# Optimization experiments

Measured on AMD Instinct MI355X. Metric: run time of the kernel, lower is better.

Reference implementation:

```python
import jax, jax.numpy as jnp
import numpy as np

N_NODES = 50000
N_EDGES = 800000
D = 128          # embed_dim
H = 8            # heads
C = D // H       # per-head channels
F = 512          # ff_hidden_dim
LN_EPS = 1e-5
NEG_SLOPE = 0.2  # PyG GATConv default negative_slope


def _layernorm(x, g, b):
    mu = jnp.mean(x, axis=-1, keepdims=True)
    var = jnp.mean(jnp.square(x - mu), axis=-1, keepdims=True)
    return (x - mu) * jax.lax.rsqrt(var + LN_EPS) * g + b


def _gat_conv(x, edge_index, W, att_src, att_dst, bias):
    # PyG GATConv (concat=True, add_self_loops=True, shared lin for src/dst)
    N = x.shape[0]
    xl = (x @ W.T).reshape(N, H, C)                 # [N,H,C]
    a_s = jnp.sum(xl * att_src, axis=-1)            # [N,H]
    a_d = jnp.sum(xl * att_dst, axis=-1)            # [N,H]
    loops = jnp.arange(N)
    src = jnp.concatenate([edge_index[0], loops])   # [E+N]
    dst = jnp.concatenate([edge_index[1], loops])
    e = jax.nn.leaky_relu(a_s[src] + a_d[dst], NEG_SLOPE)  # [E+N,H]
    # segment softmax over incoming edges per destination node
    m = jax.ops.segment_max(e, dst, num_segments=N)
    m = jnp.where(jnp.isfinite(m), m, jnp.zeros_like(m))
    ex = jnp.exp(e - m[dst])
    s = jax.ops.segment_sum(ex, dst, num_segments=N)
    alpha = ex / (s[dst] + 1e-16)                   # [E+N,H]
    msg = xl[src] * alpha[:, :, None]               # [E+N,H,C]
    out = jax.ops.segment_sum(msg, dst, num_segments=N)  # [N,H,C]
    return out.reshape(N, H * C) + bias


def setup_inputs() -> dict:
    key = jax.random.key(0)
    ks = jax.random.split(key, 12)
    sc_d = 1.0 / np.sqrt(D)
    sc_f = 1.0 / np.sqrt(F)
    return {
        "x": jax.random.normal(ks[0], (N_NODES, D), dtype=jnp.float32),
        "virtual_edge_index": jax.random.randint(ks[1], (2, N_EDGES), 0, N_NODES, dtype=jnp.int64),
        "W_gat": jax.random.normal(ks[2], (H * C, D), dtype=jnp.float32) * sc_d,
        "att_src": jax.random.normal(ks[3], (H, C), dtype=jnp.float32) * sc_d,
        "att_dst": jax.random.normal(ks[4], (H, C), dtype=jnp.float32) * sc_d,
        "bias_gat": jnp.zeros((H * C,), dtype=jnp.float32),
        "W1": jax.random.normal(ks[5], (F, D), dtype=jnp.float32) * sc_d,
        "b1": jnp.zeros((F,), dtype=jnp.float32),
        "W2": jax.random.normal(ks[6], (D, F), dtype=jnp.float32) * sc_f,
        "b2": jnp.zeros((D,), dtype=jnp.float32),
        "g1": jnp.ones((D,), dtype=jnp.float32),
        "beta1": jnp.zeros((D,), dtype=jnp.float32),
        "g2": jnp.ones((D,), dtype=jnp.float32),
        "beta2": jnp.zeros((D,), dtype=jnp.float32),
    }


def reference(x, virtual_edge_index, W_gat, att_src, att_dst, bias_gat,
              W1, b1, W2, b2, g1, beta1, g2, beta2):
    h_gat = _gat_conv(x, virtual_edge_index, W_gat, att_src, att_dst, bias_gat)
    h = _layernorm(x + h_gat, g1, beta1)
    h_ff = jax.nn.relu(h @ W1.T + b1) @ W2.T + b2
    return _layernorm(h + h_ff, g2, beta2)
```

## Files before the change

kernel.cpp:

```cpp
#include <hip/hip_runtime.h>
#include <hip/hip_bf16.h>

#define N_NODES 50000
#define N_EDGES 800000
#define N_TOT   850000
#define DIM 128
#define HEADS 8
#define CH 16
#define FF 512
#define LN_EPS 1e-5f
#define NEG_SLOPE 0.2f

typedef __bf16 bf16x8 __attribute__((ext_vector_type(8)));
typedef float f32x4 __attribute__((ext_vector_type(4)));

__device__ __forceinline__ float bfr2f(unsigned short u) {
  return __uint_as_float(((unsigned)u) << 16);
}
__device__ __forceinline__ unsigned short f2bfr(float f) {
  __hip_bfloat16 h = __float2bfloat16(f);
  return *(unsigned short*)&h;
}
__device__ __forceinline__ float bf2f(__hip_bfloat16 h) { return __bfloat162float(h); }
__device__ __forceinline__ __hip_bfloat16 f2bf(float f) { return __float2bfloat16(f); }

__device__ __forceinline__ bf16x8 ldcvt8(const float* __restrict__ p) {
  const float4 a = ((const float4*)p)[0];
  const float4 b = ((const float4*)p)[1];
  bf16x8 r;
  r[0] = (__bf16)a.x; r[1] = (__bf16)a.y; r[2] = (__bf16)a.z; r[3] = (__bf16)a.w;
  r[4] = (__bf16)b.x; r[5] = (__bf16)b.y; r[6] = (__bf16)b.z; r[7] = (__bf16)b.w;
  return r;
}
__device__ __forceinline__ void load8f(const float* __restrict__ p, float* v) {
  const float4 a = ((const float4*)p)[0];
  const float4 b = ((const float4*)p)[1];
  v[0]=a.x; v[1]=a.y; v[2]=a.z; v[3]=a.w; v[4]=b.x; v[5]=b.y; v[6]=b.z; v[7]=b.w;
}

__device__ __forceinline__ int ld_src(const int* ei, int mode, int e) {
  int v = mode ? ei[2 * e] : ei[e];
  return min(max(v, 0), N_NODES - 1);
}
__device__ __forceinline__ int ld_dst(const int* ei, int mode, int e) {
  int v = mode ? ei[2 * (N_EDGES + e)] : ei[N_EDGES + e];
  return min(max(v, 0), N_NODES - 1);
}

__global__ __launch_bounds__(256) void k_setup(const float* __restrict__ Wg,
                                               const float* __restrict__ W1,
                                               const float* __restrict__ W2,
                                               __hip_bfloat16* __restrict__ wb,
                                               const int* __restrict__ ei,
                                               int* __restrict__ flag,
                                               int* __restrict__ dz) {
  int i = blockIdx.x * 256 + threadIdx.x;
  if (i < 16384)       wb[i] = f2bf(Wg[i]);
  else if (i < 81920)  wb[i] = f2bf(W1[i - 16384]);
  else if (i < 147456) wb[i] = f2bf(W2[i - 81920]);
  if (i < 100096) dz[i] = 0;
  if (i == 0) {
    int any = 0;
    for (int k = 1; k < 64; k += 2) any |= ei[k];
    *flag = (any == 0) ? 1 : 0;
  }
}

__global__ __launch_bounds__(256) void k_xl(const float* __restrict__ x,
                                            const __hip_bfloat16* __restrict__ Wgb,
                                            __hip_bfloat16* __restrict__ xl) {
  int w = (blockIdx.x * blockDim.x + threadIdx.x) >> 6;
  if (w >= 3125 * 2) return;
  int l = threadIdx.x & 63, quad = l >> 4, r = l & 15;
  int strip = w >> 1, cc = w & 1;
  const __bf16* wb = (const __bf16*)Wgb;
  f32x4 acc[4];
#pragma unroll
  for (int t = 0; t < 4; ++t) acc[t] = (f32x4){0.f, 0.f, 0.f, 0.f};
  int arow = strip * 16 + r;
  bf16x8 af[4];
#pragma unroll
  for (int kk = 0; kk < 4; ++kk) af[kk] = ldcvt8(x + arow * DIM + kk * 32 + quad * 8);
#pragma unroll
  for (int kk = 0; kk < 4; ++kk) {
    bf16x8 bfr[4];
#pragma unroll
    for (int t = 0; t < 4; ++t)
      bfr[t] = *(const bf16x8*)(wb + (cc * 64 + t * 16 + r) * DIM + kk * 32 + quad * 8);
#pragma unroll
    for (int t = 0; t < 4; ++t)
      acc[t] = __builtin_amdgcn_mfma_f32_16x16x32_bf16(af[kk], bfr[t], acc[t], 0, 0, 0);
  }
#pragma unroll
  for (int t = 0; t < 4; ++t)
#pragma unroll
    for (int j = 0; j < 4; ++j) {
      int row = strip * 16 + quad * 4 + j;
      int col = cc * 64 + t * 16 + r;
      xl[row * DIM + col] = f2bf(acc[t][j]);
    }
}

__global__ __launch_bounds__(256) void k_score(const __hip_bfloat16* __restrict__ xl,
                                               const float* __restrict__ att_s,
                                               const float* __restrict__ att_d,
                                               float* __restrict__ a_s, float* __restrict__ a_d) {
  int t = blockIdx.x * 256 + threadIdx.x;
  if (t >= N_NODES * HEADS) return;
  int n = t >> 3, h = t & 7;
  const __hip_bfloat16* p = xl + n * DIM + h * CH;
  float s = 0.f, d = 0.f;
#pragma unroll
  for (int c = 0; c < CH; ++c) {
    float v = bf2f(p[c]);
    s += v * att_s[h * CH + c];
    d += v * att_d[h * CH + c];
  }
  a_s[t] = s; a_d[t] = d;
}

__global__ __launch_bounds__(256) void k_hist(const int* __restrict__ ei, const int* __restrict__ flag,
                                              int* __restrict__ deg) {
  int e = blockIdx.x * 256 + threadIdx.x;
  if (e < N_EDGES) atomicAdd(&deg[ld_dst(ei, *flag, e)], 1);
}

__global__ __launch_bounds__(1024) void k_scan(const int* __restrict__ deg, int* __restrict__ offs) {
  __shared__ int wtot[16];
  __shared__ int wbase[16];
  __shared__ int running_s;
  int tid = threadIdx.x, wv = tid >> 6, ln = tid & 63;
  if (tid == 0) running_s = 0;
  __syncthreads();
  for (int base = 0; base < N_NODES; base += 4096) {
    int i0 = base + tid * 4;
    int v0 = 0, v1 = 0, v2 = 0, v3 = 0;
    if (i0 + 3 < N_NODES) {
      int4 dv = *(const int4*)(deg + i0);
      v0 = dv.x + 1; v1 = dv.y + 1; v2 = dv.z + 1; v3 = dv.w + 1;
    } else {
      if (i0 + 0 < N_NODES) v0 = deg[i0 + 0] + 1;
      if (i0 + 1 < N_NODES) v1 = deg[i0 + 1] + 1;
      if (i0 + 2 < N_NODES) v2 = deg[i0 + 2] + 1;
      if (i0 + 3 < N_NODES) v3 = deg[i0 + 3] + 1;
    }
    int tt = v0 + v1 + v2 + v3;
    int xsc = tt;
#pragma unroll
    for (int off = 1; off < 64; off <<= 1) {
      int t = __shfl_up(xsc, off);
      if (ln >= off) xsc += t;
    }
    if (ln == 63) wtot[wv] = xsc;
    __syncthreads();
    if (wv == 0) {
      int t = (ln < 16) ? wtot[ln] : 0;
#pragma unroll
      for (int off = 1; off < 16; off <<= 1) {
        int u = __shfl_up(t, off);
        if (ln >= off) t += u;
      }
      if (ln < 16) wbase[ln] = t;
    }
    __syncthreads();
    int run0 = running_s;
    int excl = run0 + ((wv == 0) ? 0 : wbase[wv - 1]) + xsc - tt;
    if (i0 + 0 < N_NODES) offs[i0 + 0] = excl;
    excl += v0;
    if (i0 + 1 < N_NODES) offs[i0 + 1] = excl;
    excl += v1;
    if (i0 + 2 < N_NODES) offs[i0 + 2] = excl;
    excl += v2;
    if (i0 + 3 < N_NODES) offs[i0 + 3] = excl;
    __syncthreads();
    if (tid == 1023) running_s = run0 + wbase[15];
  }
  __syncthreads();
  if (tid == 0) offs[N_NODES] = running_s;
}

__global__ __launch_bounds__(256) void k_scatter(const int* __restrict__ ei, const int* __restrict__ flag,
                                                 const int* __restrict__ offs,
                                                 int* __restrict__ fill, int* __restrict__ eid,
                                                 int* __restrict__ did) {
  int e = blockIdx.x * 256 + threadIdx.x;
  if (e < N_NODES) { int p = offs[e]; eid[p] = e; did[p] = e; }
  if (e < N_EDGES) {
    int m = *flag;
    int d = ld_dst(ei, m, e);
    int p = offs[d] + 1 + atomicAdd(&fill[d], 1);
    eid[p] = ld_src(ei, m, e);
    did[p] = d;
  }
}

__global__ __launch_bounds__(256) void k_escore(const int* __restrict__ eid, const int* __restrict__ did,
                                                const float* __restrict__ a_s, const float* __restrict__ a_d,
                                                unsigned short* __restrict__ ex) {
  int p = blockIdx.x * 256 + threadIdx.x;
  if (p >= N_TOT) return;
  int s = eid[p], d = did[p];
  float as8[8], ad8[8];
  load8f(a_s + s * 8, as8);
  load8f(a_d + d * 8, ad8);
  unsigned int o[4];
#pragma unroll
  for (int k = 0; k < 4; ++k) {
    float v0 = as8[2 * k] + ad8[2 * k];
    v0 = v0 > 0.f ? v0 : NEG_SLOPE * v0;
    float v1 = as8[2 * k + 1] + ad8[2 * k + 1];
    v1 = v1 > 0.f ? v1 : NEG_SLOPE * v1;
    unsigned short e0 = f2bfr(__expf(v0));
    unsigned short e1 = f2bfr(__expf(v1));
    o[k] = (unsigned)e0 | ((unsigned)e1 << 16);
  }
  *(uint4*)(ex + p * 8) = make_uint4(o[0], o[1], o[2], o[3]);
}

__global__ __launch_bounds__(256) void k_attn(const int* __restrict__ eid, const int* __restrict__ offs,
                                              const unsigned short* __restrict__ ex,
                                              const __hip_bfloat16* __restrict__ xl,
                                              const float* __restrict__ x,
                                              const float* __restrict__ bias,
                                              const float* __restrict__ g1,
                                              const float* __restrict__ be1,
                                              __hip_bfloat16* __restrict__ h1out) {
  int wv = threadIdx.x >> 6, l = threadIdx.x & 63;
  int n = blockIdx.x * 4 + wv;
  int start = offs[n], end = offs[n + 1];

  float sme = 0.f;
  int flat1 = end * 8;
  for (int q = start * 8 + l; q < flat1; q += 64) sme += bfr2f(ex[q]);
  sme += __shfl_xor(sme, 8);
  sme += __shfl_xor(sme, 16);
  sme += __shfl_xor(sme, 32);
  float smh = __shfl(sme, l >> 3);
  float inv = 1.f / (smh + 1e-16f);

  int h = l >> 3;
  const unsigned short* xlu = (const unsigned short*)xl;
  float A0 = 0.f, A1 = 0.f, B0 = 0.f, B1 = 0.f, C0 = 0.f, C1 = 0.f, D0 = 0.f, D1 = 0.f;
  int p = start;
  for (; p + 4 <= end; p += 4) {
    int s0 = eid[p], s1 = eid[p + 1], s2 = eid[p + 2], s3 = eid[p + 3];
    float w0 = bfr2f(ex[(p)     * 8 + h]);
    float w1 = bfr2f(ex[(p + 1) * 8 + h]);
    float w2 = bfr2f(ex[(p + 2) * 8 + h]);
    float w3 = bfr2f(ex[(p + 3) * 8 + h]);
    ushort2 u0 = *(const ushort2*)(xlu + s0 * DIM + 2 * l);
    ushort2 u1 = *(const ushort2*)(xlu + s1 * DIM + 2 * l);
    ushort2 u2 = *(const ushort2*)(xlu + s2 * DIM + 2 * l);
    ushort2 u3 = *(const ushort2*)(xlu + s3 * DIM + 2 * l);
    A0 += w0 * bfr2f(u0.x); A1 += w0 * bfr2f(u0.y);
    B0 += w1 * bfr2f(u1.x); B1 += w1 * bfr2f(u1.y);
    C0 += w2 * bfr2f(u2.x); C1 += w2 * bfr2f(u2.y);
    D0 += w3 * bfr2f(u3.x); D1 += w3 * bfr2f(u3.y);
  }
  for (; p < end; ++p) {
    int s = eid[p];
    float wq = bfr2f(ex[p * 8 + h]);
    ushort2 u = *(const ushort2*)(xlu + s * DIM + 2 * l);
    A0 += wq * bfr2f(u.x); A1 += wq * bfr2f(u.y);
  }
  float acc0 = ((A0 + B0) + (C0 + D0)) * inv;
  float acc1 = ((A1 + B1) + (C1 + D1)) * inv;

  float2 xv = *(const float2*)(x + n * DIM + 2 * l);
  float2 bv = *(const float2*)(bias + 2 * l);
  float v0 = acc0 + bv.x + xv.x;
  float v1 = acc1 + bv.y + xv.y;
  float s2 = v0 + v1;
  for (int off = 32; off >= 1; off >>= 1) s2 += __shfl_xor(s2, off);
  float mu = s2 * (1.f / 128.f);
  float d0 = v0 - mu, d1 = v1 - mu;
  float q = d0 * d0 + d1 * d1;
  for (int off = 32; off >= 1; off >>= 1) q += __shfl_xor(q, off);
  float rs = rsqrtf(q * (1.f / 128.f) + LN_EPS);
  float2 gv = *(const float2*)(g1 + 2 * l);
  float2 bev = *(const float2*)(be1 + 2 * l);
  ushort2 o;
  o.x = f2bfr(d0 * rs * gv.x + bev.x);
  o.y = f2bfr(d1 * rs * gv.y + bev.y);
  *(ushort2*)((unsigned short*)h1out + n * DIM + 2 * l) = o;
}

#define LDSP 520
__global__ __launch_bounds__(256) void k_ffn(const __hip_bfloat16* __restrict__ h1,
                                             const __hip_bfloat16* __restrict__ W1b,
                                             const float* __restrict__ b1,
                                             const __hip_bfloat16* __restrict__ W2b,
                                             const float* __restrict__ b2,
                                             const float* __restrict__ g2,
                                             const float* __restrict__ be2,
                                             float* __restrict__ out) {
  __shared__ __bf16 hid[32 * LDSP];
  __shared__ float ps[4][2][16], pq[4][2][16];
  int wv = threadIdx.x >> 6, l = threadIdx.x & 63, quad = l >> 4, r = l & 15;
  int base = blockIdx.x * 32;
  const __bf16* h1b = (const __bf16*)h1;
  const __bf16* w1 = (const __bf16*)W1b;
  const __bf16* w2 = (const __bf16*)W2b;

  bf16x8 bn[2][4];
#pragma unroll
  for (int kk = 0; kk < 4; ++kk) {
    bn[0][kk] = *(const bf16x8*)(h1b + (base + r) * DIM + kk * 32 + quad * 8);
    bn[1][kk] = *(const bf16x8*)(h1b + (base + 16 + r) * DIM + kk * 32 + quad * 8);
  }
  f32x4 acc1[8][2];
#pragma unroll
  for (int tm = 0; tm < 8; ++tm)
#pragma unroll
    for (int tn = 0; tn < 2; ++tn) acc1[tm][tn] = (f32x4){0.f, 0.f, 0.f, 0.f};
#pragma unroll
  for (int kk = 0; kk < 4; ++kk) {
    bf16x8 wf[8];
#pragma unroll
    for (int tm = 0; tm < 8; ++tm)
      wf[tm] = *(const bf16x8*)(w1 + (wv * 128 + tm * 16 + r) * DIM + kk * 32 + quad * 8);
#pragma unroll
    for (int tm = 0; tm < 8; ++tm) {
      acc1[tm][0] = __builtin_amdgcn_mfma_f32_16x16x32_bf16(wf[tm], bn[0][kk], acc1[tm][0], 0, 0, 0);
      acc1[tm][1] = __builtin_amdgcn_mfma_f32_16x16x32_bf16(wf[tm], bn[1][kk], acc1[tm][1], 0, 0, 0);
    }
  }
#pragma unroll
  for (int tm = 0; tm < 8; ++tm) {
    int f0 = wv * 128 + tm * 16 + quad * 4;
    float4 bb = *(const float4*)(b1 + f0);
#pragma unroll
    for (int tn = 0; tn < 2; ++tn) {
      int node = tn * 16 + r;
      ushort4 o;
      o.x = f2bfr(fmaxf(acc1[tm][tn][0] + bb.x, 0.f));
      o.y = f2bfr(fmaxf(acc1[tm][tn][1] + bb.y, 0.f));
      o.z = f2bfr(fmaxf(acc1[tm][tn][2] + bb.z, 0.f));
      o.w = f2bfr(fmaxf(acc1[tm][tn][3] + bb.w, 0.f));
      *(ushort4*)&hid[node * LDSP + f0] = o;
    }
  }
  __syncthreads();

  f32x4 acc2[2][2];
#pragma unroll
  for (int s = 0; s < 2; ++s)
#pragma unroll
    for (int tn = 0; tn < 2; ++tn) acc2[s][tn] = (f32x4){0.f, 0.f, 0.f, 0.f};
#pragma unroll
  for (int k2 = 0; k2 < 8; ++k2) {
    int ka = 2 * k2, kb = 2 * k2 + 1;
    bf16x8 a0 = *(const bf16x8*)&hid[(r) * LDSP + ka * 32 + quad * 8];
    bf16x8 a1 = *(const bf16x8*)&hid[(16 + r) * LDSP + ka * 32 + quad * 8];
    bf16x8 a0b = *(const bf16x8*)&hid[(r) * LDSP + kb * 32 + quad * 8];
    bf16x8 a1b = *(const bf16x8*)&hid[(16 + r) * LDSP + kb * 32 + quad * 8];
    bf16x8 wa[2], wbq[2];
#pragma unroll
    for (int tn = 0; tn < 2; ++tn) {
      wa[tn]  = *(const bf16x8*)(w2 + (wv * 32 + tn * 16 + r) * FF + ka * 32 + quad * 8);
      wbq[tn] = *(const bf16x8*)(w2 + (wv * 32 + tn * 16 + r) * FF + kb * 32 + quad * 8);
    }
#pragma unroll
    for (int tn = 0; tn < 2; ++tn) {
      acc2[0][tn] = __builtin_amdgcn_mfma_f32_16x16x32_bf16(a0, wa[tn], acc2[0][tn], 0, 0, 0);
      acc2[1][tn] = __builtin_amdgcn_mfma_f32_16x16x32_bf16(a1, wa[tn], acc2[1][tn], 0, 0, 0);
    }
#pragma unroll
    for (int tn = 0; tn < 2; ++tn) {
      acc2[0][tn] = __builtin_amdgcn_mfma_f32_16x16x32_bf16(a0b, wbq[tn], acc2[0][tn], 0, 0, 0);
      acc2[1][tn] = __builtin_amdgcn_mfma_f32_16x16x32_bf16(a1b, wbq[tn], acc2[1][tn], 0, 0, 0);
    }
  }
#pragma unroll
  for (int s = 0; s < 2; ++s)
#pragma unroll
    for (int tn = 0; tn < 2; ++tn) {
      int col = wv * 32 + tn * 16 + r;
      float b2c = b2[col];
#pragma unroll
      for (int j = 0; j < 4; ++j)
        acc2[s][tn][j] += b2c + bf2f(h1[(base + s * 16 + quad * 4 + j) * DIM + col]);
    }
#pragma unroll
  for (int s = 0; s < 2; ++s)
#pragma unroll
    for (int j = 0; j < 4; ++j) {
      float sm = acc2[s][0][j] + acc2[s][1][j];
      float qm = acc2[s][0][j] * acc2[s][0][j] + acc2[s][1][j] * acc2[s][1][j];
      sm += __shfl_xor(sm, 1); sm += __shfl_xor(sm, 2); sm += __shfl_xor(sm, 4); sm += __shfl_xor(sm, 8);
      qm += __shfl_xor(qm, 1); qm += __shfl_xor(qm, 2); qm += __shfl_xor(qm, 4); qm += __shfl_xor(qm, 8);
      if (r == j) { ps[wv][s][quad * 4 + j] = sm; pq[wv][s][quad * 4 + j] = qm; }
    }
  __syncthreads();
#pragma unroll
  for (int s = 0; s < 2; ++s)
#pragma unroll
    for (int j = 0; j < 4; ++j) {
      int row16 = quad * 4 + j;
      float st = (ps[0][s][row16] + ps[1][s][row16]) + (ps[2][s][row16] + ps[3][s][row16]);
      float qt = (pq[0][s][row16] + pq[1][s][row16]) + (pq[2][s][row16] + pq[3][s][row16]);
      float mu = st * (1.f / 128.f);
      float var = qt * (1.f / 128.f) - mu * mu;
      float rs = rsqrtf(var + LN_EPS);
      int grow = base + s * 16 + row16;
      if (grow < N_NODES) {
#pragma unroll
        for (int tn = 0; tn < 2; ++tn) {
          int col = wv * 32 + tn * 16 + r;
          out[grow * DIM + col] = (acc2[s][tn][j] - mu) * rs * g2[col] + be2[col];
        }
      }
    }
}

#define OFF_XL     0u
#define SZ_XL      (N_NODES * DIM * 2u)
#define OFF_AS     (OFF_XL + SZ_XL)
#define SZ_AS      (N_NODES * HEADS * 4u)
#define OFF_AD     (OFF_AS + SZ_AS)
#define OFF_DEG    (OFF_AD + SZ_AS)
#define SZ_DEG     200192u
#define OFF_FILL   (OFF_DEG + SZ_DEG)
#define OFF_OFFS   (OFF_FILL + SZ_DEG)
#define SZ_OFFS    200448u
#define OFF_FLAG   (OFF_OFFS + SZ_OFFS)
#define OFF_EID    (OFF_FLAG + 256u)
#define SZ_EID     3400192u
#define OFF_DID    (OFF_EID + SZ_EID)
#define OFF_EX     (OFF_DID + SZ_EID)
#define SZ_EX      13600768u
#define OFF_H1     (OFF_EX + SZ_EX)
#define SZ_H1      (50016u * DIM * 2u)
#define OFF_WB     (OFF_H1 + SZ_H1)

extern "C" void kernel_launch(void* const* d_in, const int* in_sizes, int n_in,
                              void* d_out, int out_size, void* d_ws, size_t ws_size,
                              hipStream_t stream) {
  const float* x     = (const float*)d_in[0];
  const int*   ei    = (const int*)d_in[1];
  const float* Wg    = (const float*)d_in[2];
  const float* att_s = (const float*)d_in[3];
  const float* att_d = (const float*)d_in[4];
  const float* bias  = (const float*)d_in[5];
  const float* W1    = (const float*)d_in[6];
  const float* b1    = (const float*)d_in[7];
  const float* W2    = (const float*)d_in[8];
  const float* b2    = (const float*)d_in[9];
  const float* g1    = (const float*)d_in[10];
  const float* be1   = (const float*)d_in[11];
  const float* g2    = (const float*)d_in[12];
  const float* be2   = (const float*)d_in[13];

  char* ws = (char*)d_ws;
  __hip_bfloat16* xl     = (__hip_bfloat16*)(ws + OFF_XL);
  float*          a_s    = (float*)(ws + OFF_AS);
  float*          a_d    = (float*)(ws + OFF_AD);
  int*            deg    = (int*)(ws + OFF_DEG);
  int*            fill   = (int*)(ws + OFF_FILL);
  int*            offs   = (int*)(ws + OFF_OFFS);
  int*            flag   = (int*)(ws + OFF_FLAG);
  int*            eid    = (int*)(ws + OFF_EID);
  int*            did    = (int*)(ws + OFF_DID);
  unsigned short* ex     = (unsigned short*)(ws + OFF_EX);
  __hip_bfloat16* h1     = (__hip_bfloat16*)(ws + OFF_H1);
  __hip_bfloat16* wbuf   = (__hip_bfloat16*)(ws + OFF_WB);
  __hip_bfloat16* Wgb    = wbuf;
  __hip_bfloat16* W1b    = wbuf + 16384;
  __hip_bfloat16* W2b    = wbuf + 81920;
  float*          out    = (float*)d_out;

  k_setup  <<<576,   256, 0, stream>>>(Wg, W1, W2, wbuf, ei, flag, deg);
  k_xl     <<<1563,  256, 0, stream>>>(x, Wgb, xl);
  k_score  <<<1563,  256, 0, stream>>>(xl, att_s, att_d, a_s, a_d);
  k_hist   <<<3125,  256, 0, stream>>>(ei, flag, deg);
  k_scan   <<<1,    1024, 0, stream>>>(deg, offs);
  k_scatter<<<3125,  256, 0, stream>>>(ei, flag, offs, fill, eid, did);
  k_escore <<<3321,  256, 0, stream>>>(eid, did, a_s, a_d, ex);
  k_attn   <<<12500, 256, 0, stream>>>(eid, offs, ex, xl, x, bias, g1, be1, h1);
  k_ffn    <<<1563,  256, 0, stream>>>(h1, W1b, b1, W2b, b2, g2, be2, out);
}
```

Before: 361.3 us.

## Split fused FFN into two kernels with global MFMA-fragment-layout hidden buffer

Splits the fused FFN kernel into an up-projection kernel that writes the ReLU hidden activations to a global scratch buffer (reusing the xl region) in a layout pre-swizzled for MFMA operand fragments, and a down-projection plus LayerNorm kernel that reads them back. Processing runs in two row chunks so the hidden buffer fits in the reused space. It also zero-fills the padded tail rows of h1. This removes the large LDS footprint and the block barrier to raise occupancy, at the cost of extra global memory traffic for the 512-wide hidden tensor and additional kernel launches.

```diff
diff --git a/kernel.cpp b/kernel.cpp
--- a/kernel.cpp
+++ b/kernel.cpp
@@ -53,12 +53,14 @@
                                                __hip_bfloat16* __restrict__ wb,
                                                const int* __restrict__ ei,
                                                int* __restrict__ flag,
-                                               int* __restrict__ dz) {
+                                               int* __restrict__ dz,
+                                               __hip_bfloat16* __restrict__ h1) {
   int i = blockIdx.x * 256 + threadIdx.x;
   if (i < 16384)       wb[i] = f2bf(Wg[i]);
   else if (i < 81920)  wb[i] = f2bf(W1[i - 16384]);
   else if (i < 147456) wb[i] = f2bf(W2[i - 81920]);
   if (i < 100096) dz[i] = 0;
+  if (i < 1024) ((int*)(h1 + 50000 * DIM))[i] = 0;
   if (i == 0) {
     int any = 0;
     for (int k = 1; k < 64; k += 2) any |= ei[k];
@@ -285,22 +287,16 @@
   *(ushort2*)((unsigned short*)h1out + n * DIM + 2 * l) = o;
 }
 
-#define LDSP 520
-__global__ __launch_bounds__(256) void k_ffn(const __hip_bfloat16* __restrict__ h1,
-                                             const __hip_bfloat16* __restrict__ W1b,
-                                             const float* __restrict__ b1,
-                                             const __hip_bfloat16* __restrict__ W2b,
-                                             const float* __restrict__ b2,
-                                             const float* __restrict__ g2,
-                                             const float* __restrict__ be2,
-                                             float* __restrict__ out) {
-  __shared__ __bf16 hid[32 * LDSP];
-  __shared__ float ps[4][2][16], pq[4][2][16];
+__global__ __launch_bounds__(256) void k_ffn1(const __hip_bfloat16* __restrict__ h1,
+                                              const __hip_bfloat16* __restrict__ W1b,
+                                              const float* __restrict__ b1,
+                                              __hip_bfloat16* __restrict__ hid,
+                                              int row_base) {
   int wv = threadIdx.x >> 6, l = threadIdx.x & 63, quad = l >> 4, r = l & 15;
-  int base = blockIdx.x * 32;
+  int blk = blockIdx.x;
+  int base = row_base + blk * 32;
   const __bf16* h1b = (const __bf16*)h1;
   const __bf16* w1 = (const __bf16*)W1b;
-  const __bf16* w2 = (const __bf16*)W2b;
 
   bf16x8 bn[2][4];
 #pragma unroll
@@ -325,51 +321,60 @@
       acc1[tm][1] = __builtin_amdgcn_mfma_f32_16x16x32_bf16(wf[tm], bn[1][kk], acc1[tm][1], 0, 0, 0);
     }
   }
+  unsigned short* hb = (unsigned short*)hid;
 #pragma unroll
   for (int tm = 0; tm < 8; ++tm) {
     int f0 = wv * 128 + tm * 16 + quad * 4;
     float4 bb = *(const float4*)(b1 + f0);
 #pragma unroll
     for (int tn = 0; tn < 2; ++tn) {
-      int node = tn * 16 + r;
       ushort4 o;
       o.x = f2bfr(fmaxf(acc1[tm][tn][0] + bb.x, 0.f));
       o.y = f2bfr(fmaxf(acc1[tm][tn][1] + bb.y, 0.f));
       o.z = f2bfr(fmaxf(acc1[tm][tn][2] + bb.z, 0.f));
       o.w = f2bfr(fmaxf(acc1[tm][tn][3] + bb.w, 0.f));
-      *(ushort4*)&hid[node * LDSP + f0] = o;
-    }
-  }
-  __syncthreads();
+      int idx = ((blk * 2 + tn) * 64 + wv * 16 + tm * 2 + (quad >> 1)) * 128
+                + r * 8 + (quad & 1) * 4;
+      *(ushort4*)(hb + idx) = o;
+    }
+  }
+}
+
+__global__ __launch_bounds__(256) void k_ffn2(const __hip_bfloat16* __restrict__ hid,
+                                              const __hip_bfloat16* __restrict__ W2b,
+                                              const float* __restrict__ b2,
+                                              const float* __restrict__ g2,
+                                              const float* __restrict__ be2,
+                                              const __hip_bfloat16* __restrict__ h1,
+                                              float* __restrict__ out,
+                                              int row_base) {
+  __shared__ float ps[4][2][16], pq[4][2][16];
+  int wv = threadIdx.x >> 6, l = threadIdx.x & 63, quad = l >> 4, r = l & 15;
+  int blk = blockIdx.x;
+  int base = row_base + blk * 32;
+  const __bf16* w2 = (const __bf16*)W2b;
+  const unsigned short* hb = (const unsigned short*)hid;
 
   f32x4 acc2[2][2];
 #pragma unroll
   for (int s = 0; s < 2; ++s)
 #pragma unroll
     for (int tn = 0; tn < 2; ++tn) acc2[s][tn] = (f32x4){0.f, 0.f, 0.f, 0.f};
-#pragma unroll
-  for (int k2 = 0; k2 < 8; ++k2) {
-    int ka = 2 * k2, kb = 2 * k2 + 1;
-    bf16x8 a0 = *(const bf16x8*)&hid[(r) * LDSP + ka * 32 + quad * 8];
-    bf16x8 a1 = *(const bf16x8*)&hid[(16 + r) * LDSP + ka * 32 + quad * 8];
-    bf16x8 a0b = *(const bf16x8*)&hid[(r) * LDSP + kb * 32 + quad * 8];
-    bf16x8 a1b = *(const bf16x8*)&hid[(16 + r) * LDSP + kb * 32 + quad * 8];
-    bf16x8 wa[2], wbq[2];
-#pragma unroll
-    for (int tn = 0; tn < 2; ++tn) {
-      wa[tn]  = *(const bf16x8*)(w2 + (wv * 32 + tn * 16 + r) * FF + ka * 32 + quad * 8);
-      wbq[tn] = *(const bf16x8*)(w2 + (wv * 32 + tn * 16 + r) * FF + kb * 32 + quad * 8);
-    }
-#pragma unroll
-    for (int tn = 0; tn < 2; ++tn) {
-      acc2[0][tn] = __builtin_amdgcn_mfma_f32_16x16x32_bf16(a0, wa[tn], acc2[0][tn], 0, 0, 0);
-      acc2[1][tn] = __builtin_amdgcn_mfma_f32_16x16x32_bf16(a1, wa[tn], acc2[1][tn], 0, 0, 0);
-    }
-#pragma unroll
-    for (int tn = 0; tn < 2; ++tn) {
-      acc2[0][tn] = __builtin_amdgcn_mfma_f32_16x16x32_bf16(a0b, wbq[tn], acc2[0][tn], 0, 0, 0);
-      acc2[1][tn] = __builtin_amdgcn_mfma_f32_16x16x32_bf16(a1b, wbq[tn], acc2[1][tn], 0, 0, 0);
-    }
+
+  const unsigned short* a0base = hb + ((blk * 2 + 0) * 64 + quad) * 128 + r * 8;
+  const unsigned short* a1base = hb + ((blk * 2 + 1) * 64 + quad) * 128 + r * 8;
+  const __bf16* w2base = w2 + (wv * 32 + r) * FF + quad * 8;
+
+#pragma unroll 4
+  for (int ka = 0; ka < 16; ++ka) {
+    bf16x8 a0 = *(const bf16x8*)(a0base + ka * 512);
+    bf16x8 a1 = *(const bf16x8*)(a1base + ka * 512);
+    bf16x8 wa0 = *(const bf16x8*)(w2base + ka * 32);
+    bf16x8 wa1 = *(const bf16x8*)(w2base + 16 * FF + ka * 32);
+    acc2[0][0] = __builtin_amdgcn_mfma_f32_16x16x32_bf16(a0, wa0, acc2[0][0], 0, 0, 0);
+    acc2[0][1] = __builtin_amdgcn_mfma_f32_16x16x32_bf16(a0, wa1, acc2[0][1], 0, 0, 0);
+    acc2[1][0] = __builtin_amdgcn_mfma_f32_16x16x32_bf16(a1, wa0, acc2[1][0], 0, 0, 0);
+    acc2[1][1] = __builtin_amdgcn_mfma_f32_16x16x32_bf16(a1, wa1, acc2[1][1], 0, 0, 0);
   }
 #pragma unroll
   for (int s = 0; s < 2; ++s)
@@ -432,6 +437,9 @@
 #define OFF_H1     (OFF_EX + SZ_EX)
 #define SZ_H1      (50016u * DIM * 2u)
 #define OFF_WB     (OFF_H1 + SZ_H1)
+#define FFN_CHUNK0_BLOCKS 782
+#define FFN_CHUNK1_BLOCKS 781
+#define FFN_CHUNK0_ROWS   (FFN_CHUNK0_BLOCKS * 32)
 
 extern "C" void kernel_launch(void* const* d_in, const int* in_sizes, int n_in,
                               void* d_out, int out_size, void* d_ws, size_t ws_size,
@@ -467,9 +475,10 @@
   __hip_bfloat16* Wgb    = wbuf;
   __hip_bfloat16* W1b    = wbuf + 16384;
   __hip_bfloat16* W2b    = wbuf + 81920;
+  __hip_bfloat16* hid    = (__hip_bfloat16*)(ws + OFF_XL);
   float*          out    = (float*)d_out;
 
-  k_setup  <<<576,   256, 0, stream>>>(Wg, W1, W2, wbuf, ei, flag, deg);
+  k_setup  <<<576,   256, 0, stream>>>(Wg, W1, W2, wbuf, ei, flag, deg, h1);
   k_xl     <<<1563,  256, 0, stream>>>(x, Wgb, xl);
   k_score  <<<1563,  256, 0, stream>>>(xl, att_s, att_d, a_s, a_d);
   k_hist   <<<3125,  256, 0, stream>>>(ei, flag, deg);
@@ -477,5 +486,8 @@
   k_scatter<<<3125,  256, 0, stream>>>(ei, flag, offs, fill, eid, did);
   k_escore <<<3321,  256, 0, stream>>>(eid, did, a_s, a_d, ex);
   k_attn   <<<12500, 256, 0, stream>>>(eid, offs, ex, xl, x, bias, g1, be1, h1);
-  k_ffn    <<<1563,  256, 0, stream>>>(h1, W1b, b1, W2b, b2, g2, be2, out);
-}
+  k_ffn1   <<<FFN_CHUNK0_BLOCKS, 256, 0, stream>>>(h1, W1b, b1, hid, 0);
+  k_ffn2   <<<FFN_CHUNK0_BLOCKS, 256, 0, stream>>>(hid, W2b, b2, g2, be2, h1, out, 0);
+  k_ffn1   <<<FFN_CHUNK1_BLOCKS, 256, 0, stream>>>(h1, W1b, b1, hid, FFN_CHUNK0_ROWS);
+  k_ffn2   <<<FFN_CHUNK1_BLOCKS, 256, 0, stream>>>(hid, W2b, b2, g2, be2, h1, out, FFN_CHUNK0_ROWS);
+}
```

Result: slower. 375.7 us (+4.0%).
